# Kernel optimization log

Measured on AMD Instinct MI355X. Metric: run time of the kernel, lower is better.

The kernel has to match this reference:

```python
import jax, jax.numpy as jnp
import numpy as np

N = 100_000          # nodes
E = 1_600_000        # edges (avg degree 16)
IN_C, OUT_C = 256, 128


def setup_inputs() -> dict:
    key = jax.random.key(0)
    k1, k2, k3, k4, k5 = jax.random.split(key, 5)
    X = jax.random.normal(k1, (N, IN_C), dtype=jnp.float32)
    # nn.Linear(in, out, bias=False) weight has shape [out, in]
    W = jax.random.normal(k2, (OUT_C, IN_C), dtype=jnp.float32) * (1.0 / np.sqrt(IN_C))
    A_rows = jnp.sort(jax.random.randint(k3, (E,), 0, N, dtype=jnp.int32))
    A_cols = jax.random.randint(k4, (E,), 0, N, dtype=jnp.int32)
    # positive values mimicking symmetric-normalized adjacency entries
    A_vals = jax.random.uniform(k5, (E,), dtype=jnp.float32) * (1.0 / 16.0)
    return {"X": X, "W": W, "A_rows": A_rows, "A_cols": A_cols, "A_vals": A_vals}


def reference(X, W, A_rows, A_cols, A_vals):
    # X = self._linear(X)  ->  X @ W^T   [N, OUT_C]
    H = jnp.einsum("ni,oi->no", X, W)
    # X = torch.sparse.mm(A_hat, X): out[r] += v * H[c] for each edge (r, c, v)
    msgs = A_vals[:, None] * H[A_cols]                      # [E, OUT_C]
    out = jax.ops.segment_sum(msgs, A_rows, num_segments=N)  # [N, OUT_C]
    return out
```

## Files before the change

kernel.cpp:

```cpp
#include <hip/hip_runtime.h>
#include <hip/hip_bf16.h>

#define NNODES 100000
#define NEDGES 1600000
#define IN_C   256
#define OUT_C  128

typedef short bf16x8 __attribute__((ext_vector_type(8)));
typedef float f32x4  __attribute__((ext_vector_type(4)));

static __device__ __forceinline__ unsigned short f2bf(float f) {
    union { float f; unsigned u; } c; c.f = f;
    unsigned r = c.u + 0x7fffu + ((c.u >> 16) & 1u);
    return (unsigned short)(r >> 16);
}
static __device__ __forceinline__ float bflo(unsigned u) {
    union { unsigned u; float f; } c; c.u = u << 16; return c.f;
}
static __device__ __forceinline__ float bfhi(unsigned u) {
    union { unsigned u; float f; } c; c.u = u & 0xffff0000u; return c.f;
}

union BF8 { bf16x8 v; unsigned short s[8]; };

__global__ __launch_bounds__(512, 4) void gemm_xwt(const float* __restrict__ X,
                                                   const float* __restrict__ W,
                                                   unsigned short* __restrict__ H) {
    __shared__ unsigned short Wsh[128 * 256];

    const int tid  = threadIdx.x;
    const int lane = tid & 63;
    const int wid  = tid >> 6;

#pragma unroll
    for (int p = 0; p < 16; ++p) {
        int idx = p * 512 + tid;
        int n   = idx >> 6;
        int c4  = idx & 63;
        float4 v = *(const float4*)(W + (size_t)n * IN_C + c4 * 4);
        int byte = (n * 512 + c4 * 8) ^ ((n & 7) << 4);
        *(ushort4*)((char*)Wsh + byte) =
            make_ushort4(f2bf(v.x), f2bf(v.y), f2bf(v.z), f2bf(v.w));
    }
    __syncthreads();

    const int r0   = blockIdx.x * 128 + wid * 16;
    int arow = r0 + (lane & 15);
    if (arow > NNODES - 1) arow = NNODES - 1;
    const float* xrow = X + (size_t)arow * IN_C + (lane >> 4) * 8;

    f32x4 acc[8] = {};
#pragma unroll
    for (int ks = 0; ks < 8; ++ks) {
        float4 a0 = *(const float4*)(xrow + ks * 32);
        float4 a1 = *(const float4*)(xrow + ks * 32 + 4);
        BF8 t;
        t.s[0] = f2bf(a0.x); t.s[1] = f2bf(a0.y); t.s[2] = f2bf(a0.z); t.s[3] = f2bf(a0.w);
        t.s[4] = f2bf(a1.x); t.s[5] = f2bf(a1.y); t.s[6] = f2bf(a1.z); t.s[7] = f2bf(a1.w);
        const int kb = ks * 64 + (lane >> 4) * 16;
#pragma unroll
        for (int n8 = 0; n8 < 8; ++n8) {
            int nr   = n8 * 16 + (lane & 15);
            int byte = (nr * 512 + kb) ^ ((nr & 7) << 4);
            bf16x8 b = *(const bf16x8*)((const char*)Wsh + byte);
            acc[n8] = __builtin_amdgcn_mfma_f32_16x16x32_bf16(t.v, b, acc[n8],
                                                              0, 0, 0);
        }
    }

#pragma unroll
    for (int n8 = 0; n8 < 8; ++n8) {
#pragma unroll
        for (int r = 0; r < 4; ++r) {
            int grow = r0 + (lane >> 4) * 4 + r;
            if (grow < NNODES)
                H[(size_t)grow * OUT_C + n8 * 16 + (lane & 15)] = f2bf(acc[n8][r]);
        }
    }
}

__global__ __launch_bounds__(256) void build_rowptr(const int* __restrict__ rows,
                                                    int* __restrict__ rowptr) {
    int r = blockIdx.x * 256 + threadIdx.x;
    if (r > NNODES) return;
    int lo = 0, hi = NEDGES;
    while (lo < hi) {
        int mid = (lo + hi) >> 1;
        if (rows[mid] < r) lo = mid + 1; else hi = mid;
    }
    rowptr[r] = lo;
}

__global__ __launch_bounds__(256) void spmm_rows(const uint4* __restrict__ H4,
                                                 const int* __restrict__ rowptr,
                                                 const int* __restrict__ cols,
                                                 const float* __restrict__ vals,
                                                 float* __restrict__ out) {
    const int wid  = threadIdx.x >> 6;
    const int lane = threadIdx.x & 63;
    const int row  = blockIdx.x * 4 + wid;
    if (row >= NNODES) return;

    const int s  = rowptr[row];
    const int e  = rowptr[row + 1];
    const int g  = lane >> 4;
    const int cg = lane & 15;

    float acc[8];
#pragma unroll
    for (int t = 0; t < 8; ++t) acc[t] = 0.f;

    for (int base = s; base < e; base += 64) {
        const int cnt = (e - base < 64) ? (e - base) : 64;
        int   ec = 0;
        float ev = 0.f;
        if (lane < cnt) { ec = cols[base + lane]; ev = vals[base + lane]; }

        int j = 0;
        for (; j + 16 <= cnt; j += 16) {
#pragma unroll
            for (int q = 0; q < 4; ++q) {
                int   c = __shfl(ec, j + q * 4 + g);
                float v = __shfl(ev, j + q * 4 + g);
                uint4 u = H4[(size_t)c * 16 + cg];
                acc[0] += v * bflo(u.x); acc[1] += v * bfhi(u.x);
                acc[2] += v * bflo(u.y); acc[3] += v * bfhi(u.y);
                acc[4] += v * bflo(u.z); acc[5] += v * bfhi(u.z);
                acc[6] += v * bflo(u.w); acc[7] += v * bfhi(u.w);
            }
        }
        for (; j < cnt; j += 4) {
            int   c = __shfl(ec, j + g);
            float v = __shfl(ev, j + g);
            uint4 u = H4[(size_t)c * 16 + cg];
            acc[0] += v * bflo(u.x); acc[1] += v * bfhi(u.x);
            acc[2] += v * bflo(u.y); acc[3] += v * bfhi(u.y);
            acc[4] += v * bflo(u.z); acc[5] += v * bfhi(u.z);
            acc[6] += v * bflo(u.w); acc[7] += v * bfhi(u.w);
        }
    }

#pragma unroll
    for (int t = 0; t < 8; ++t) {
        acc[t] += __shfl_xor(acc[t], 16);
        acc[t] += __shfl_xor(acc[t], 32);
    }
    if (lane < 16) {
        float4 v0 = make_float4(acc[0], acc[1], acc[2], acc[3]);
        float4 v1 = make_float4(acc[4], acc[5], acc[6], acc[7]);
        *(float4*)(out + (size_t)row * OUT_C + cg * 8)     = v0;
        *(float4*)(out + (size_t)row * OUT_C + cg * 8 + 4) = v1;
    }
}

extern "C" void kernel_launch(void* const* d_in, const int* in_sizes, int n_in,
                              void* d_out, int out_size, void* d_ws, size_t ws_size,
                              hipStream_t stream) {
    const float* X      = (const float*)d_in[0];
    const float* W      = (const float*)d_in[1];
    const int*   A_rows = (const int*)d_in[2];
    const int*   A_cols = (const int*)d_in[3];
    const float* A_vals = (const float*)d_in[4];
    float* out = (float*)d_out;

    unsigned short* H   = (unsigned short*)d_ws;
    int* rowptr = (int*)((char*)d_ws +
                         (size_t)NNODES * OUT_C * sizeof(unsigned short));

    gemm_xwt<<<(NNODES + 127) / 128, 512, 0, stream>>>(X, W, H);
    build_rowptr<<<(NNODES + 1 + 255) / 256, 256, 0, stream>>>(A_rows, rowptr);
    spmm_rows<<<(NNODES + 3) / 4, 256, 0, stream>>>((const uint4*)H, rowptr,
                                                    A_cols, A_vals, out);
}
```

Before: 101.5 us.

## Map one row per 16-lane group in SpMM instead of one row per wavefront

The SpMM kernel now assigns each 16-lane quarter of a wavefront to its own output row, so a wave processes four rows at once rather than splitting one row's edges across four groups. This removes the cross-group shuffle reduction and the idle lanes on the final store, and it issues four times fewer blocks. In exchange, the four rows in a wave can have different degrees, so lanes diverge and the loop runs as long as the longest row. Edge metadata is loaded in chunks of 32 per group, and the grid assumes NNODES is divisible by 16, with no bounds check.

```diff
diff --git a/kernel.cpp b/kernel.cpp
--- a/kernel.cpp
+++ b/kernel.cpp
@@ -96,42 +96,43 @@
                                                  const int* __restrict__ cols,
                                                  const float* __restrict__ vals,
                                                  float* __restrict__ out) {
+    const int lane = threadIdx.x & 63;
     const int wid  = threadIdx.x >> 6;
-    const int lane = threadIdx.x & 63;
-    const int row  = blockIdx.x * 4 + wid;
-    if (row >= NNODES) return;
+    const int g    = lane >> 4;
+    const int cg   = lane & 15;
+    const int glb  = g << 4;
+    const int row  = (blockIdx.x * 4 + wid) * 4 + g;
 
-    const int s  = rowptr[row];
-    const int e  = rowptr[row + 1];
-    const int g  = lane >> 4;
-    const int cg = lane & 15;
+    const int s = rowptr[row];
+    const int e = rowptr[row + 1];
 
     float acc[8];
 #pragma unroll
     for (int t = 0; t < 8; ++t) acc[t] = 0.f;
 
-    for (int base = s; base < e; base += 64) {
-        const int cnt = (e - base < 64) ? (e - base) : 64;
-        int   ec = 0;
-        float ev = 0.f;
-        if (lane < cnt) { ec = cols[base + lane]; ev = vals[base + lane]; }
+    for (int base = s; base < e; base += 32) {
+        const int rem = e - base;
+        const int cnt = rem < 32 ? rem : 32;
+        int ec0 = 0, ec1 = 0;
+        float ev0 = 0.f, ev1 = 0.f;
+        if (cg < cnt)      { ec0 = cols[base + cg];      ev0 = vals[base + cg]; }
+        if (cg + 16 < cnt) { ec1 = cols[base + 16 + cg]; ev1 = vals[base + 16 + cg]; }
 
-        int j = 0;
-        for (; j + 16 <= cnt; j += 16) {
-#pragma unroll
-            for (int q = 0; q < 4; ++q) {
-                int   c = __shfl(ec, j + q * 4 + g);
-                float v = __shfl(ev, j + q * 4 + g);
-                uint4 u = H4[(size_t)c * 16 + cg];
-                acc[0] += v * bflo(u.x); acc[1] += v * bfhi(u.x);
-                acc[2] += v * bflo(u.y); acc[3] += v * bfhi(u.y);
-                acc[4] += v * bflo(u.z); acc[5] += v * bfhi(u.z);
-                acc[6] += v * bflo(u.w); acc[7] += v * bfhi(u.w);
-            }
+        const int c1 = cnt < 16 ? cnt : 16;
+#pragma unroll 4
+        for (int j = 0; j < c1; ++j) {
+            int   c = __shfl(ec0, glb + j);
+            float v = __shfl(ev0, glb + j);
+            uint4 u = H4[(size_t)c * 16 + cg];
+            acc[0] += v * bflo(u.x); acc[1] += v * bfhi(u.x);
+            acc[2] += v * bflo(u.y); acc[3] += v * bfhi(u.y);
+            acc[4] += v * bflo(u.z); acc[5] += v * bfhi(u.z);
+            acc[6] += v * bflo(u.w); acc[7] += v * bfhi(u.w);
         }
-        for (; j < cnt; j += 4) {
-            int   c = __shfl(ec, j + g);
-            float v = __shfl(ev, j + g);
+#pragma unroll 4
+        for (int j = 16; j < cnt; ++j) {
+            int   c = __shfl(ec1, glb + j - 16);
+            float v = __shfl(ev1, glb + j - 16);
             uint4 u = H4[(size_t)c * 16 + cg];
             acc[0] += v * bflo(u.x); acc[1] += v * bfhi(u.x);
             acc[2] += v * bflo(u.y); acc[3] += v * bfhi(u.y);
@@ -140,17 +141,10 @@
         }
     }
 
-#pragma unroll
-    for (int t = 0; t < 8; ++t) {
-        acc[t] += __shfl_xor(acc[t], 16);
-        acc[t] += __shfl_xor(acc[t], 32);
-    }
-    if (lane < 16) {
-        float4 v0 = make_float4(acc[0], acc[1], acc[2], acc[3]);
-        float4 v1 = make_float4(acc[4], acc[5], acc[6], acc[7]);
-        *(float4*)(out + (size_t)row * OUT_C + cg * 8)     = v0;
-        *(float4*)(out + (size_t)row * OUT_C + cg * 8 + 4) = v1;
-    }
+    float4 v0 = make_float4(acc[0], acc[1], acc[2], acc[3]);
+    float4 v1 = make_float4(acc[4], acc[5], acc[6], acc[7]);
+    *(float4*)(out + (size_t)row * OUT_C + cg * 8)     = v0;
+    *(float4*)(out + (size_t)row * OUT_C + cg * 8 + 4) = v1;
 }
 
 extern "C" void kernel_launch(void* const* d_in, const int* in_sizes, int n_in,
@@ -169,6 +163,6 @@
 
     gemm_xwt<<<(NNODES + 127) / 128, 512, 0, stream>>>(X, W, H);
     build_rowptr<<<(NNODES + 1 + 255) / 256, 256, 0, stream>>>(A_rows, rowptr);
-    spmm_rows<<<(NNODES + 3) / 4, 256, 0, stream>>>((const uint4*)H, rowptr,
-                                                    A_cols, A_vals, out);
+    spmm_rows<<<NNODES / 16, 256, 0, stream>>>((const uint4*)H, rowptr,
+                                               A_cols, A_vals, out);
 }
```

New measurement: 104.8 us. 3.2% more time.

## Quantize intermediate H to int8 with per-row scale for the SpMM gather

Applied to the files above, without the earlier changes.

The GEMM epilogue now computes a per-row absmax, stores H as int8 with one float scale per node, and the SpMM gathers 8-byte int8 chunks instead of 16-byte bf16 chunks. The per-row scale is folded into each edge value when the edge is loaded. The aim is to halve the random-gather traffic, which dominates the SpMM. It costs extra quantization error relative to bf16, plus an additional scale gather per edge. Output stores also become nontemporal.

```diff
diff --git a/kernel.cpp b/kernel.cpp
--- a/kernel.cpp
+++ b/kernel.cpp
@@ -14,18 +14,13 @@
     unsigned r = c.u + 0x7fffu + ((c.u >> 16) & 1u);
     return (unsigned short)(r >> 16);
 }
-static __device__ __forceinline__ float bflo(unsigned u) {
-    union { unsigned u; float f; } c; c.u = u << 16; return c.f;
-}
-static __device__ __forceinline__ float bfhi(unsigned u) {
-    union { unsigned u; float f; } c; c.u = u & 0xffff0000u; return c.f;
-}
 
 union BF8 { bf16x8 v; unsigned short s[8]; };
 
 __global__ __launch_bounds__(512, 4) void gemm_xwt(const float* __restrict__ X,
                                                    const float* __restrict__ W,
-                                                   unsigned short* __restrict__ H) {
+                                                   signed char* __restrict__ H8,
+                                                   float* __restrict__ scale) {
     __shared__ unsigned short Wsh[128 * 256];
 
     const int tid  = threadIdx.x;
@@ -68,13 +63,33 @@
         }
     }
 
-#pragma unroll
-    for (int n8 = 0; n8 < 8; ++n8) {
-#pragma unroll
-        for (int r = 0; r < 4; ++r) {
-            int grow = r0 + (lane >> 4) * 4 + r;
-            if (grow < NNODES)
-                H[(size_t)grow * OUT_C + n8 * 16 + (lane & 15)] = f2bf(acc[n8][r]);
+    float amax[4];
+#pragma unroll
+    for (int r = 0; r < 4; ++r) {
+        float m = 0.f;
+#pragma unroll
+        for (int n8 = 0; n8 < 8; ++n8) m = fmaxf(m, fabsf(acc[n8][r]));
+        amax[r] = m;
+    }
+#pragma unroll
+    for (int d = 1; d < 16; d <<= 1)
+#pragma unroll
+        for (int r = 0; r < 4; ++r)
+            amax[r] = fmaxf(amax[r], __shfl_xor(amax[r], d));
+
+#pragma unroll
+    for (int r = 0; r < 4; ++r) {
+        int grow = r0 + (lane >> 4) * 4 + r;
+        if (grow < NNODES) {
+            float am  = amax[r];
+            float inv = am > 0.f ? 127.f / am : 0.f;
+            if ((lane & 15) == 0) scale[grow] = am * (1.f / 127.f);
+#pragma unroll
+            for (int n8 = 0; n8 < 8; ++n8) {
+                float q = rintf(acc[n8][r] * inv);
+                q = fminf(127.f, fmaxf(-127.f, q));
+                H8[(size_t)grow * OUT_C + n8 * 16 + (lane & 15)] = (signed char)q;
+            }
         }
     }
 }
@@ -91,10 +106,11 @@
     rowptr[r] = lo;
 }
 
-__global__ __launch_bounds__(256) void spmm_rows(const uint4* __restrict__ H4,
+__global__ __launch_bounds__(256) void spmm_rows(const uint2* __restrict__ H2,
                                                  const int* __restrict__ rowptr,
                                                  const int* __restrict__ cols,
                                                  const float* __restrict__ vals,
+                                                 const float* __restrict__ scale,
                                                  float* __restrict__ out) {
     const int wid  = threadIdx.x >> 6;
     const int lane = threadIdx.x & 63;
@@ -114,7 +130,10 @@
         const int cnt = (e - base < 64) ? (e - base) : 64;
         int   ec = 0;
         float ev = 0.f;
-        if (lane < cnt) { ec = cols[base + lane]; ev = vals[base + lane]; }
+        if (lane < cnt) {
+            ec = cols[base + lane];
+            ev = vals[base + lane] * scale[ec];
+        }
 
         int j = 0;
         for (; j + 16 <= cnt; j += 16) {
@@ -122,21 +141,29 @@
             for (int q = 0; q < 4; ++q) {
                 int   c = __shfl(ec, j + q * 4 + g);
                 float v = __shfl(ev, j + q * 4 + g);
-                uint4 u = H4[(size_t)c * 16 + cg];
-                acc[0] += v * bflo(u.x); acc[1] += v * bfhi(u.x);
-                acc[2] += v * bflo(u.y); acc[3] += v * bfhi(u.y);
-                acc[4] += v * bflo(u.z); acc[5] += v * bfhi(u.z);
-                acc[6] += v * bflo(u.w); acc[7] += v * bfhi(u.w);
+                uint2 u = H2[(size_t)c * 16 + cg];
+                acc[0] += v * (float)(signed char)(u.x);
+                acc[1] += v * (float)(signed char)(u.x >> 8);
+                acc[2] += v * (float)(signed char)(u.x >> 16);
+                acc[3] += v * (float)(signed char)(u.x >> 24);
+                acc[4] += v * (float)(signed char)(u.y);
+                acc[5] += v * (float)(signed char)(u.y >> 8);
+                acc[6] += v * (float)(signed char)(u.y >> 16);
+                acc[7] += v * (float)(signed char)(u.y >> 24);
             }
         }
         for (; j < cnt; j += 4) {
             int   c = __shfl(ec, j + g);
             float v = __shfl(ev, j + g);
-            uint4 u = H4[(size_t)c * 16 + cg];
-            acc[0] += v * bflo(u.x); acc[1] += v * bfhi(u.x);
-            acc[2] += v * bflo(u.y); acc[3] += v * bfhi(u.y);
-            acc[4] += v * bflo(u.z); acc[5] += v * bfhi(u.z);
-            acc[6] += v * bflo(u.w); acc[7] += v * bfhi(u.w);
+            uint2 u = H2[(size_t)c * 16 + cg];
+            acc[0] += v * (float)(signed char)(u.x);
+            acc[1] += v * (float)(signed char)(u.x >> 8);
+            acc[2] += v * (float)(signed char)(u.x >> 16);
+            acc[3] += v * (float)(signed char)(u.x >> 24);
+            acc[4] += v * (float)(signed char)(u.y);
+            acc[5] += v * (float)(signed char)(u.y >> 8);
+            acc[6] += v * (float)(signed char)(u.y >> 16);
+            acc[7] += v * (float)(signed char)(u.y >> 24);
         }
     }
 
@@ -146,10 +173,10 @@
         acc[t] += __shfl_xor(acc[t], 32);
     }
     if (lane < 16) {
-        float4 v0 = make_float4(acc[0], acc[1], acc[2], acc[3]);
-        float4 v1 = make_float4(acc[4], acc[5], acc[6], acc[7]);
-        *(float4*)(out + (size_t)row * OUT_C + cg * 8)     = v0;
-        *(float4*)(out + (size_t)row * OUT_C + cg * 8 + 4) = v1;
+        f32x4 v0 = { acc[0], acc[1], acc[2], acc[3] };
+        f32x4 v1 = { acc[4], acc[5], acc[6], acc[7] };
+        __builtin_nontemporal_store(v0, (f32x4*)(out + (size_t)row * OUT_C + cg * 8));
+        __builtin_nontemporal_store(v1, (f32x4*)(out + (size_t)row * OUT_C + cg * 8 + 4));
     }
 }
 
@@ -163,12 +190,12 @@
     const float* A_vals = (const float*)d_in[4];
     float* out = (float*)d_out;
 
-    unsigned short* H   = (unsigned short*)d_ws;
-    int* rowptr = (int*)((char*)d_ws +
-                         (size_t)NNODES * OUT_C * sizeof(unsigned short));
-
-    gemm_xwt<<<(NNODES + 127) / 128, 512, 0, stream>>>(X, W, H);
+    signed char* H8    = (signed char*)d_ws;
+    float*       scale = (float*)((char*)d_ws + (size_t)NNODES * OUT_C);
+    int*         rowptr = (int*)((char*)scale + (size_t)NNODES * sizeof(float));
+
+    gemm_xwt<<<(NNODES + 127) / 128, 512, 0, stream>>>(X, W, H8, scale);
     build_rowptr<<<(NNODES + 1 + 255) / 256, 256, 0, stream>>>(A_rows, rowptr);
-    spmm_rows<<<(NNODES + 3) / 4, 256, 0, stream>>>((const uint4*)H, rowptr,
-                                                    A_cols, A_vals, out);
-}
+    spmm_rows<<<(NNODES + 3) / 4, 256, 0, stream>>>((const uint2*)H8, rowptr,
+                                                    A_cols, A_vals, scale, out);
+}
```

After: 92.15 us. 1.1x faster.
